# Optimization experiments

Hardware: AMD Instinct MI355X
Metric: run time of the kernel (lower is better)

## Reference

```python
import jax, jax.numpy as jnp
import numpy as np

V_ORIG = 32000   # original embedding vocab
V_NEW = 8000     # reparameterized vocab (size of down/up stacks and index_mapping)
D = 1024         # embedding dim
R = 16           # low-rank dim
N = 16384        # number of indices looked up


def setup_inputs() -> dict:
    key = jax.random.key(0)
    k1, k2, k3, k4, k5 = jax.random.split(key, 5)
    indices = jax.random.randint(k1, (N,), 0, V_NEW, dtype=jnp.int64)
    # index_mapping: dict new_index -> original_index, materialized as a lookup array
    index_map = jax.random.randint(k2, (V_NEW,), 0, V_ORIG, dtype=jnp.int64)
    emb_weight = jax.random.normal(k3, (V_ORIG, D), dtype=jnp.float32) * 0.02
    down = jax.random.normal(k4, (V_NEW, D, R), dtype=jnp.float32) * (1.0 / np.sqrt(D))
    up = jax.random.normal(k5, (V_NEW, R, D), dtype=jnp.float32) * (1.0 / np.sqrt(R))
    return {"indices": indices, "index_map": index_map,
            "emb_weight": emb_weight, "down": down, "up": up}


def reference(indices, index_map, emb_weight, down, up):
    # Gather original embeddings via the index mapping: [N, D]
    e = emb_weight[index_map[indices]]
    # Per-index low-rank projection: ([1,D] @ [D,R]) @ [R,D], batched over N
    h = jnp.einsum('nd,ndr->nr', e, down[indices])        # [N, R]
    out = jnp.einsum('nr,nrd->nd', h, up[indices])        # [N, D]
    # Original stacks per-index [1, D] results -> [N, 1, D]
    return out[:, None, :]
```

## Files before the change

kernel.cpp:

```cpp
#include <hip/hip_runtime.h>
#include <hip/hip_bf16.h>


#define DDIM 1024
#define RDIM 16


__global__ __launch_bounds__(256) void zero_kernel(int* p, int n) {
    int i = blockIdx.x * 256 + threadIdx.x;
    if (i < n) p[i] = 0;
}

__global__ __launch_bounds__(256) void hist_kernel(const int* __restrict__ idx,
                                                   int* __restrict__ counts, int n) {
    int i = blockIdx.x * 256 + threadIdx.x;
    if (i < n) atomicAdd(&counts[idx[i]], 1);
}

__global__ __launch_bounds__(1024) void scan_kernel(const int* __restrict__ counts,
                                                    int* __restrict__ offsets, int V) {
    __shared__ int part[1024];
    const int t = threadIdx.x;
    const int per = (V + 1023) / 1024;
    const int lo = t * per;
    const int hi = min(lo + per, V);
    int s = 0;
    for (int i = lo; i < hi; ++i) s += counts[i];
    part[t] = s;
    __syncthreads();
    for (int d = 1; d < 1024; d <<= 1) {
        int val = (t >= d) ? part[t - d] : 0;
        __syncthreads();
        part[t] += val;
        __syncthreads();
    }
    int run = (t == 0) ? 0 : part[t - 1];
    for (int i = lo; i < hi; ++i) {
        run += counts[i];
        offsets[i + 1] = run;
    }
    if (t == 0) offsets[0] = 0;
}

__global__ __launch_bounds__(256) void scatter_kernel(const int* __restrict__ idx,
                                                      const int* __restrict__ offsets,
                                                      int* __restrict__ cursor,
                                                      int* __restrict__ lists, int n) {
    int i = blockIdx.x * 256 + threadIdx.x;
    if (i < n) {
        int v = idx[i];
        int p = offsets[v] + atomicAdd(&cursor[v], 1);
        lists[p] = i;
    }
}

__global__ __launch_bounds__(256) void rows_csr_kernel(
    const int* __restrict__ index_map,
    const float* __restrict__ emb,
    const float* __restrict__ down,
    const float* __restrict__ up,
    const int* __restrict__ offsets,
    const int* __restrict__ lists,
    float* __restrict__ out)
{
    const int v   = blockIdx.x;
    const int off = offsets[v];
    const int cnt = offsets[v + 1] - off;
    if (cnt == 0) return;

    const int tid = threadIdx.x;
    const float* __restrict__ e  = emb  + (size_t)index_map[v] * DDIM;
    const float* __restrict__ dn = down + (size_t)v * (DDIM * RDIM);
    const float* __restrict__ u  = up   + (size_t)v * (RDIM * DDIM);

    const int rq   = (tid & 3) * 4;
    const int dgrp = tid >> 2;
    float4 hp = make_float4(0.f, 0.f, 0.f, 0.f);
    #pragma unroll
    for (int k = 0; k < 16; ++k) {
        const int d = dgrp + (k << 6);
        const float ed = e[d];
        float4 q = *(const float4*)(dn + (size_t)d * RDIM + rq);
        hp.x += ed * q.x;
        hp.y += ed * q.y;
        hp.z += ed * q.z;
        hp.w += ed * q.w;
    }
    #pragma unroll
    for (int m = 4; m < 64; m <<= 1) {
        hp.x += __shfl_xor(hp.x, m, 64);
        hp.y += __shfl_xor(hp.y, m, 64);
        hp.z += __shfl_xor(hp.z, m, 64);
        hp.w += __shfl_xor(hp.w, m, 64);
    }
    __shared__ float hs[4][RDIM];
    const int lane = tid & 63, wid = tid >> 6;
    if (lane < 4) {
        hs[wid][rq + 0] = hp.x;
        hs[wid][rq + 1] = hp.y;
        hs[wid][rq + 2] = hp.z;
        hs[wid][rq + 3] = hp.w;
    }
    __syncthreads();
    float hf[RDIM];
    #pragma unroll
    for (int r = 0; r < RDIM; ++r)
        hf[r] = hs[0][r] + hs[1][r] + hs[2][r] + hs[3][r];

    float4 acc = make_float4(0.f, 0.f, 0.f, 0.f);
    #pragma unroll
    for (int r = 0; r < RDIM; ++r) {
        float4 uv = *(const float4*)(u + (size_t)r * DDIM + tid * 4);
        acc.x += hf[r] * uv.x;
        acc.y += hf[r] * uv.y;
        acc.z += hf[r] * uv.z;
        acc.w += hf[r] * uv.w;
    }

    for (int j = 0; j < cnt; ++j) {
        const int n = lists[off + j];
        *(float4*)(out + (size_t)n * DDIM + tid * 4) = acc;
    }
}

__global__ __launch_bounds__(256) void rows_direct_kernel(
    const int* __restrict__ indices,
    const int* __restrict__ index_map,
    const float* __restrict__ emb,
    const float* __restrict__ down,
    const float* __restrict__ up,
    float* __restrict__ out)
{
    const int n   = blockIdx.x;
    const int v   = indices[n];
    const int tid = threadIdx.x;
    const float* __restrict__ e  = emb  + (size_t)index_map[v] * DDIM;
    const float* __restrict__ dn = down + (size_t)v * (DDIM * RDIM);
    const float* __restrict__ u  = up   + (size_t)v * (RDIM * DDIM);

    const int rq   = (tid & 3) * 4;
    const int dgrp = tid >> 2;
    float4 hp = make_float4(0.f, 0.f, 0.f, 0.f);
    #pragma unroll
    for (int k = 0; k < 16; ++k) {
        const int d = dgrp + (k << 6);
        const float ed = e[d];
        float4 q = *(const float4*)(dn + (size_t)d * RDIM + rq);
        hp.x += ed * q.x; hp.y += ed * q.y; hp.z += ed * q.z; hp.w += ed * q.w;
    }
    #pragma unroll
    for (int m = 4; m < 64; m <<= 1) {
        hp.x += __shfl_xor(hp.x, m, 64);
        hp.y += __shfl_xor(hp.y, m, 64);
        hp.z += __shfl_xor(hp.z, m, 64);
        hp.w += __shfl_xor(hp.w, m, 64);
    }
    __shared__ float hs[4][RDIM];
    const int lane = tid & 63, wid = tid >> 6;
    if (lane < 4) {
        hs[wid][rq + 0] = hp.x; hs[wid][rq + 1] = hp.y;
        hs[wid][rq + 2] = hp.z; hs[wid][rq + 3] = hp.w;
    }
    __syncthreads();
    float hf[RDIM];
    #pragma unroll
    for (int r = 0; r < RDIM; ++r)
        hf[r] = hs[0][r] + hs[1][r] + hs[2][r] + hs[3][r];

    float4 acc = make_float4(0.f, 0.f, 0.f, 0.f);
    #pragma unroll
    for (int r = 0; r < RDIM; ++r) {
        float4 uv = *(const float4*)(u + (size_t)r * DDIM + tid * 4);
        acc.x += hf[r] * uv.x; acc.y += hf[r] * uv.y;
        acc.z += hf[r] * uv.z; acc.w += hf[r] * uv.w;
    }
    *(float4*)(out + (size_t)n * DDIM + tid * 4) = acc;
}

extern "C" void kernel_launch(void* const* d_in, const int* in_sizes, int n_in,
                              void* d_out, int out_size, void* d_ws, size_t ws_size,
                              hipStream_t stream)
{
    const int*   indices   = (const int*)d_in[0];
    const int*   index_map = (const int*)d_in[1];
    const float* emb       = (const float*)d_in[2];
    const float* down      = (const float*)d_in[3];
    const float* up        = (const float*)d_in[4];
    float*       out       = (float*)d_out;

    const int N = in_sizes[0];
    const int V = in_sizes[1];

    const size_t ws_need = (size_t)(2 * V + (V + 1) + N) * sizeof(int);

    if (ws_size >= ws_need) {
        int* counts  = (int*)d_ws;
        int* cursor  = counts + V;
        int* offsets = cursor + V;
        int* lists   = offsets + (V + 1);

        zero_kernel<<<(2 * V + 255) / 256, 256, 0, stream>>>(counts, 2 * V);
        hist_kernel<<<(N + 255) / 256, 256, 0, stream>>>(indices, counts, N);
        scan_kernel<<<1, 1024, 0, stream>>>(counts, offsets, V);
        scatter_kernel<<<(N + 255) / 256, 256, 0, stream>>>(indices, offsets, cursor, lists, N);
        rows_csr_kernel<<<V, 256, 0, stream>>>(index_map, emb, down, up, offsets, lists, out);
    } else {
        rows_direct_kernel<<<N, 256, 0, stream>>>(indices, index_map, emb, down, up, out);
    }
}
```

Measured before the change: 224.3 us.

## Replace CSR bucketing with atomic linked lists and prefetch all row loads

Replaces the five-kernel histogram/scan/scatter CSR grouping with a two-kernel linked-list build, using atomicExch on a per-vocab head plus a next array. This removes the serial single-block scan and one extra pass, cutting launch count and preprocessing latency. The row kernels now issue all down, embedding and up loads up front into registers before computing, to raise memory-level parallelism. In exchange they use more registers, and the output write loop follows a dependent pointer chain.

```diff
diff --git a/kernel.cpp b/kernel.cpp
--- a/kernel.cpp
+++ b/kernel.cpp
@@ -5,86 +5,59 @@
 #define DDIM 1024
 #define RDIM 16
 
-
-__global__ __launch_bounds__(256) void zero_kernel(int* p, int n) {
-    int i = blockIdx.x * 256 + threadIdx.x;
-    if (i < n) p[i] = 0;
+__global__ __launch_bounds__(256) void init_head_kernel(int* __restrict__ head, int V) {
+    int v = blockIdx.x * 256 + threadIdx.x;
+    if (v < V) head[v] = -1;
 }
 
-__global__ __launch_bounds__(256) void hist_kernel(const int* __restrict__ idx,
-                                                   int* __restrict__ counts, int n) {
+__global__ __launch_bounds__(256) void link_kernel(const int* __restrict__ idx,
+                                                   int* __restrict__ head,
+                                                   int* __restrict__ next, int n) {
     int i = blockIdx.x * 256 + threadIdx.x;
-    if (i < n) atomicAdd(&counts[idx[i]], 1);
+    if (i < n) next[i] = atomicExch(&head[idx[i]], i);
 }
 
-__global__ __launch_bounds__(1024) void scan_kernel(const int* __restrict__ counts,
-                                                    int* __restrict__ offsets, int V) {
-    __shared__ int part[1024];
-    const int t = threadIdx.x;
-    const int per = (V + 1023) / 1024;
-    const int lo = t * per;
-    const int hi = min(lo + per, V);
-    int s = 0;
-    for (int i = lo; i < hi; ++i) s += counts[i];
-    part[t] = s;
-    __syncthreads();
-    for (int d = 1; d < 1024; d <<= 1) {
-        int val = (t >= d) ? part[t - d] : 0;
-        __syncthreads();
-        part[t] += val;
-        __syncthreads();
-    }
-    int run = (t == 0) ? 0 : part[t - 1];
-    for (int i = lo; i < hi; ++i) {
-        run += counts[i];
-        offsets[i + 1] = run;
-    }
-    if (t == 0) offsets[0] = 0;
-}
-
-__global__ __launch_bounds__(256) void scatter_kernel(const int* __restrict__ idx,
-                                                      const int* __restrict__ offsets,
-                                                      int* __restrict__ cursor,
-                                                      int* __restrict__ lists, int n) {
-    int i = blockIdx.x * 256 + threadIdx.x;
-    if (i < n) {
-        int v = idx[i];
-        int p = offsets[v] + atomicAdd(&cursor[v], 1);
-        lists[p] = i;
-    }
-}
-
-__global__ __launch_bounds__(256) void rows_csr_kernel(
+__global__ __launch_bounds__(256) void rows_ll_kernel(
     const int* __restrict__ index_map,
     const float* __restrict__ emb,
     const float* __restrict__ down,
     const float* __restrict__ up,
-    const int* __restrict__ offsets,
-    const int* __restrict__ lists,
+    const int* __restrict__ head,
+    const int* __restrict__ next,
     float* __restrict__ out)
 {
-    const int v   = blockIdx.x;
-    const int off = offsets[v];
-    const int cnt = offsets[v + 1] - off;
-    if (cnt == 0) return;
+    const int v = blockIdx.x;
+    int n0 = head[v];
+    if (n0 < 0) return;
 
-    const int tid = threadIdx.x;
+    const int tid  = threadIdx.x;
     const float* __restrict__ e  = emb  + (size_t)index_map[v] * DDIM;
     const float* __restrict__ dn = down + (size_t)v * (DDIM * RDIM);
     const float* __restrict__ u  = up   + (size_t)v * (RDIM * DDIM);
 
     const int rq   = (tid & 3) * 4;
     const int dgrp = tid >> 2;
+
+    float4 dq[16];
+    float  ev[16];
+    #pragma unroll
+    for (int k = 0; k < 16; ++k) {
+        const int d = dgrp + (k << 6);
+        dq[k] = *(const float4*)(dn + (size_t)d * RDIM + rq);
+        ev[k] = e[d];
+    }
+    float4 uvec[RDIM];
+    #pragma unroll
+    for (int r = 0; r < RDIM; ++r)
+        uvec[r] = *(const float4*)(u + (size_t)r * DDIM + tid * 4);
+
     float4 hp = make_float4(0.f, 0.f, 0.f, 0.f);
     #pragma unroll
     for (int k = 0; k < 16; ++k) {
-        const int d = dgrp + (k << 6);
-        const float ed = e[d];
-        float4 q = *(const float4*)(dn + (size_t)d * RDIM + rq);
-        hp.x += ed * q.x;
-        hp.y += ed * q.y;
-        hp.z += ed * q.z;
-        hp.w += ed * q.w;
+        hp.x += ev[k] * dq[k].x;
+        hp.y += ev[k] * dq[k].y;
+        hp.z += ev[k] * dq[k].z;
+        hp.w += ev[k] * dq[k].w;
     }
     #pragma unroll
     for (int m = 4; m < 64; m <<= 1) {
@@ -110,16 +83,16 @@
     float4 acc = make_float4(0.f, 0.f, 0.f, 0.f);
     #pragma unroll
     for (int r = 0; r < RDIM; ++r) {
-        float4 uv = *(const float4*)(u + (size_t)r * DDIM + tid * 4);
-        acc.x += hf[r] * uv.x;
-        acc.y += hf[r] * uv.y;
-        acc.z += hf[r] * uv.z;
-        acc.w += hf[r] * uv.w;
+        acc.x += hf[r] * uvec[r].x;
+        acc.y += hf[r] * uvec[r].y;
+        acc.z += hf[r] * uvec[r].z;
+        acc.w += hf[r] * uvec[r].w;
     }
 
-    for (int j = 0; j < cnt; ++j) {
-        const int n = lists[off + j];
+    int n = n0;
+    while (n >= 0) {
         *(float4*)(out + (size_t)n * DDIM + tid * 4) = acc;
+        n = next[n];
     }
 }
 
@@ -131,8 +104,8 @@
     const float* __restrict__ up,
     float* __restrict__ out)
 {
-    const int n   = blockIdx.x;
-    const int v   = indices[n];
+    const int nn  = blockIdx.x;
+    const int v   = indices[nn];
     const int tid = threadIdx.x;
     const float* __restrict__ e  = emb  + (size_t)index_map[v] * DDIM;
     const float* __restrict__ dn = down + (size_t)v * (DDIM * RDIM);
@@ -140,13 +113,24 @@
 
     const int rq   = (tid & 3) * 4;
     const int dgrp = tid >> 2;
+    float4 dq[16];
+    float  ev[16];
+    #pragma unroll
+    for (int k = 0; k < 16; ++k) {
+        const int d = dgrp + (k << 6);
+        dq[k] = *(const float4*)(dn + (size_t)d * RDIM + rq);
+        ev[k] = e[d];
+    }
+    float4 uvec[RDIM];
+    #pragma unroll
+    for (int r = 0; r < RDIM; ++r)
+        uvec[r] = *(const float4*)(u + (size_t)r * DDIM + tid * 4);
+
     float4 hp = make_float4(0.f, 0.f, 0.f, 0.f);
     #pragma unroll
     for (int k = 0; k < 16; ++k) {
-        const int d = dgrp + (k << 6);
-        const float ed = e[d];
-        float4 q = *(const float4*)(dn + (size_t)d * RDIM + rq);
-        hp.x += ed * q.x; hp.y += ed * q.y; hp.z += ed * q.z; hp.w += ed * q.w;
+        hp.x += ev[k] * dq[k].x; hp.y += ev[k] * dq[k].y;
+        hp.z += ev[k] * dq[k].z; hp.w += ev[k] * dq[k].w;
     }
     #pragma unroll
     for (int m = 4; m < 64; m <<= 1) {
@@ -170,11 +154,10 @@
     float4 acc = make_float4(0.f, 0.f, 0.f, 0.f);
     #pragma unroll
     for (int r = 0; r < RDIM; ++r) {
-        float4 uv = *(const float4*)(u + (size_t)r * DDIM + tid * 4);
-        acc.x += hf[r] * uv.x; acc.y += hf[r] * uv.y;
-        acc.z += hf[r] * uv.z; acc.w += hf[r] * uv.w;
+        acc.x += hf[r] * uvec[r].x; acc.y += hf[r] * uvec[r].y;
+        acc.z += hf[r] * uvec[r].z; acc.w += hf[r] * uvec[r].w;
     }
-    *(float4*)(out + (size_t)n * DDIM + tid * 4) = acc;
+    *(float4*)(out + (size_t)nn * DDIM + tid * 4) = acc;
 }
 
 extern "C" void kernel_launch(void* const* d_in, const int* in_sizes, int n_in,
@@ -191,19 +174,14 @@
     const int N = in_sizes[0];
     const int V = in_sizes[1];
 
-    const size_t ws_need = (size_t)(2 * V + (V + 1) + N) * sizeof(int);
+    const size_t ws_need = (size_t)(V + N) * sizeof(int);
 
     if (ws_size >= ws_need) {
-        int* counts  = (int*)d_ws;
-        int* cursor  = counts + V;
-        int* offsets = cursor + V;
-        int* lists   = offsets + (V + 1);
-
-        zero_kernel<<<(2 * V + 255) / 256, 256, 0, stream>>>(counts, 2 * V);
-        hist_kernel<<<(N + 255) / 256, 256, 0, stream>>>(indices, counts, N);
-        scan_kernel<<<1, 1024, 0, stream>>>(counts, offsets, V);
-        scatter_kernel<<<(N + 255) / 256, 256, 0, stream>>>(indices, offsets, cursor, lists, N);
-        rows_csr_kernel<<<V, 256, 0, stream>>>(index_map, emb, down, up, offsets, lists, out);
+        int* head = (int*)d_ws;
+        int* next = head + V;
+        init_head_kernel<<<(V + 255) / 256, 256, 0, stream>>>(head, V);
+        link_kernel<<<(N + 255) / 256, 256, 0, stream>>>(indices, head, next, N);
+        rows_ll_kernel<<<V, 256, 0, stream>>>(index_map, emb, down, up, head, next, out);
     } else {
         rows_direct_kernel<<<N, 256, 0, stream>>>(indices, index_map, emb, down, up, out);
     }
```

Result: faster. 214.6 us (-4.3%).
